# Kernel tuning notes

Hardware: AMD Instinct MI355X
Metric: run time of the kernel (lower is better)

The kernel has to match this reference:

```python
import jax, jax.numpy as jnp
import numpy as np

B, L, D_MODEL = 2, 2048, 512
EXPAND = 2
ED = EXPAND * D_MODEL          # d_inner = 1024
N = 16                          # d_state
D_CONV = 4
DT_RANK = (D_MODEL + N - 1) // N  # 32
D_FF = 1024
EPS = 1e-5


def _mamba_params(key, pre):
    ks = jax.random.split(key, 6)
    s = 0.02
    p = {}
    p[pre + 'in_w'] = jax.random.normal(ks[0], (D_MODEL, 2 * ED), jnp.float32) * s
    p[pre + 'conv_w'] = jax.random.normal(ks[1], (ED, 1, D_CONV), jnp.float32) * s
    p[pre + 'conv_b'] = jnp.zeros((ED,), jnp.float32)
    p[pre + 'xproj_w'] = jax.random.normal(ks[2], (ED, DT_RANK + 2 * N), jnp.float32) * s
    p[pre + 'dt_w'] = jax.random.normal(ks[3], (DT_RANK, ED), jnp.float32) * s
    p[pre + 'dt_b'] = jax.random.normal(ks[4], (ED,), jnp.float32) * s
    # S4D-real init: A_log = log(1..N) per channel
    p[pre + 'A_log'] = jnp.log(jnp.broadcast_to(jnp.arange(1, N + 1, dtype=jnp.float32), (ED, N)))
    p[pre + 'D'] = jnp.ones((ED,), jnp.float32)
    p[pre + 'out_w'] = jax.random.normal(ks[5], (ED, D_MODEL), jnp.float32) * s
    return p


def setup_inputs() -> dict:
    key = jax.random.key(0)
    k_x, k_f, k_b, k_ffn = jax.random.split(key, 4)
    inp = {'x': jax.random.normal(k_x, (B, L, D_MODEL), jnp.float32)}
    inp.update(_mamba_params(k_f, 'f_'))
    inp.update(_mamba_params(k_b, 'b_'))
    inp['norm1_g'] = jnp.ones((D_MODEL,), jnp.float32)
    inp['norm1_b'] = jnp.zeros((D_MODEL,), jnp.float32)
    inp['norm2_g'] = jnp.ones((D_MODEL,), jnp.float32)
    inp['norm2_b'] = jnp.zeros((D_MODEL,), jnp.float32)
    k1, k2 = jax.random.split(k_ffn)
    inp['ffn_w1'] = jax.random.normal(k1, (D_MODEL, D_FF), jnp.float32) * 0.02
    inp['ffn_b1'] = jnp.zeros((D_FF,), jnp.float32)
    inp['ffn_w2'] = jax.random.normal(k2, (D_FF, D_MODEL), jnp.float32) * 0.02
    inp['ffn_b2'] = jnp.zeros((D_MODEL,), jnp.float32)
    return inp


def _selective_scan(x, delta, A, Bm, C, Dp):
    # x, delta: (B,L,ED); A: (ED,N); Bm, C: (B,L,N); Dp: (ED,)
    def step(h, inp):
        x_t, d_t, B_t, C_t = inp  # (B,ED),(B,ED),(B,N),(B,N)
        dA = jnp.exp(d_t[..., None] * A)                      # (B,ED,N)
        dBx = (d_t * x_t)[..., None] * B_t[:, None, :]        # (B,ED,N)
        h = dA * h + dBx
        y = jnp.einsum('ben,bn->be', h, C_t)
        return h, y

    h0 = jnp.zeros((x.shape[0], ED, N), x.dtype)
    xs = (x.transpose(1, 0, 2), delta.transpose(1, 0, 2),
          Bm.transpose(1, 0, 2), C.transpose(1, 0, 2))
    _, ys = jax.lax.scan(step, h0, xs)
    return ys.transpose(1, 0, 2) + x * Dp


def _mamba(x, in_w, conv_w, conv_b, xproj_w, dt_w, dt_b, A_log, Dp, out_w):
    xz = x @ in_w                                  # (B,L,2*ED)
    xs, z = jnp.split(xz, 2, axis=-1)
    # depthwise causal conv over time
    xc = jax.lax.conv_general_dilated(
        xs.transpose(0, 2, 1), conv_w, (1,), [(D_CONV - 1, 0)],
        dimension_numbers=('NCH', 'OIH', 'NCH'), feature_group_count=ED)
    xc = jax.nn.silu(xc.transpose(0, 2, 1) + conv_b)          # (B,L,ED)
    dbl = xc @ xproj_w                                        # (B,L,DT_RANK+2N)
    dt = dbl[..., :DT_RANK]
    Bm = dbl[..., DT_RANK:DT_RANK + N]
    C = dbl[..., DT_RANK + N:]
    delta = jax.nn.softplus(dt @ dt_w + dt_b)                 # (B,L,ED)
    A = -jnp.exp(A_log)
    y = _selective_scan(xc, delta, A, Bm, C, Dp)
    y = y * jax.nn.silu(z)
    return y @ out_w


def _layernorm(h, g, b):
    mu = jnp.mean(h, axis=-1, keepdims=True)
    var = jnp.var(h, axis=-1, keepdims=True)
    return (h - mu) * jax.lax.rsqrt(var + EPS) * g + b


def _ffn(h, w1, b1, w2, b2):
    return jnp.maximum(h @ w1 + b1, 0.0) @ w2 + b2


def reference(x,
              f_in_w, f_conv_w, f_conv_b, f_xproj_w, f_dt_w, f_dt_b, f_A_log, f_D, f_out_w,
              b_in_w, b_conv_w, b_conv_b, b_xproj_w, b_dt_w, b_dt_b, b_A_log, b_D, b_out_w,
              norm1_g, norm1_b, norm2_g, norm2_b,
              ffn_w1, ffn_b1, ffn_w2, ffn_b2):
    mf = _mamba(x, f_in_w, f_conv_w, f_conv_b, f_xproj_w, f_dt_w, f_dt_b, f_A_log, f_D, f_out_w)
    mf = _layernorm(mf, norm1_g, norm1_b)
    out_f = _ffn(mf, ffn_w1, ffn_b1, ffn_w2, ffn_b2) + mf
    # NOTE: original code computes norm2 but then uses the UN-normalized
    # backward output (variable shadowing bug); we replicate that faithfully.
    mb = _mamba(jnp.flip(x, axis=1), b_in_w, b_conv_w, b_conv_b, b_xproj_w,
                b_dt_w, b_dt_b, b_A_log, b_D, b_out_w)
    out_b = _ffn(mb, ffn_w1, ffn_b1, ffn_w2, ffn_b2) + mb
    return out_f + out_b
```

## Files before the change

### kernel.cpp

```cpp
#include <hip/hip_runtime.h>
#include <hip/hip_bf16.h>
#include <math.h>


#define BD 2
#define LD 2048
#define DMODEL 512
#define EDIM 1024
#define NST 16
#define DTR 32
#define DFF 1024
#define MROWS (BD*LD)

typedef __hip_bfloat16 bf16;
typedef __bf16 bf16x8 __attribute__((ext_vector_type(8)));
typedef __bf16 bf16x4 __attribute__((ext_vector_type(4)));
typedef float  f32x4  __attribute__((ext_vector_type(4)));

__device__ __forceinline__ float sig_(float x) { return 1.f / (1.f + __expf(-x)); }

__device__ __forceinline__ void glds16(const void* g, void* l)
{
    __builtin_amdgcn_global_load_lds(
        (const __attribute__((address_space(1))) void*)g,
        (__attribute__((address_space(3))) void*)l, 16, 0, 0);
}

__global__ __launch_bounds__(256)
void prep_k(const float* __restrict__ x, bf16* __restrict__ xbf,
            const float* __restrict__ inw_f, const float* __restrict__ inw_b,
            bf16* __restrict__ inwT,
            const float* __restrict__ outw_f, const float* __restrict__ outw_b,
            bf16* __restrict__ outwT,
            const float* __restrict__ fw1, bf16* __restrict__ fw1T,
            const float* __restrict__ fw2, bf16* __restrict__ fw2T,
            const float* __restrict__ xp_f, const float* __restrict__ xp_b,
            bf16* __restrict__ xpT,
            const float* __restrict__ dtw_f, const float* __restrict__ dtw_b,
            bf16* __restrict__ dtwT)
{
    const int bid = blockIdx.x, tid = threadIdx.x;
    if (bid < 2048) {
        size_t i = (size_t)bid * 1024 + tid * 4;
        float4 v = *(const float4*)(x + i);
        bf16* o = xbf + i;
        o[0] = __float2bfloat16(v.x); o[1] = __float2bfloat16(v.y);
        o[2] = __float2bfloat16(v.z); o[3] = __float2bfloat16(v.w);
        return;
    }
    const float* W; bf16* WT; int R, C, cx, ry;
    if (bid < 4096) {
        int d = (bid - 2048) >> 10, t = (bid - 2048) & 1023;
        W = d ? inw_b : inw_f; WT = inwT + (size_t)d * 2048 * 512;
        R = 512; C = 2048; cx = t & 63; ry = t >> 6;
    } else if (bid < 5120) {
        int d = (bid - 4096) >> 9, t = (bid - 4096) & 511;
        W = d ? outw_b : outw_f; WT = outwT + (size_t)d * 512 * 1024;
        R = 1024; C = 512; cx = t & 15; ry = t >> 4;
    } else if (bid < 5632) {
        int t = bid - 5120; W = fw1; WT = fw1T; R = 512; C = 1024;
        cx = t & 31; ry = t >> 5;
    } else if (bid < 6144) {
        int t = bid - 5632; W = fw2; WT = fw2T; R = 1024; C = 512;
        cx = t & 15; ry = t >> 4;
    } else if (bid < 6272) {
        int d = (bid - 6144) >> 6, t = (bid - 6144) & 63;
        W = d ? xp_b : xp_f; WT = xpT + (size_t)d * 64 * 1024;
        R = 1024; C = 64; cx = t & 1; ry = t >> 1;
    } else {
        int d = (bid - 6272) >> 5, t = (bid - 6272) & 31;
        W = d ? dtw_b : dtw_f; WT = dtwT + (size_t)d * 1024 * DTR;
        R = 32; C = 1024; cx = t; ry = 0;
    }
    __shared__ float tt[32][33];
    const int c0 = cx * 32, r0 = ry * 32;
    const int col = tid & 31, rr = tid >> 5;
#pragma unroll
    for (int p = 0; p < 4; ++p)
        tt[p * 8 + rr][col] = W[(size_t)(r0 + p * 8 + rr) * C + c0 + col];
    __syncthreads();
#pragma unroll
    for (int p = 0; p < 4; ++p)
        WT[(size_t)(c0 + p * 8 + rr) * R + r0 + col] =
            __float2bfloat16(tt[col][p * 8 + rr]);
}

template<int BN, int MODE, bool FLIPD1, bool CATK>
__global__ __launch_bounds__(256)
void bgemm3_k(const bf16* __restrict__ A, size_t Astr, int lda,
              const bf16* __restrict__ BT, size_t Bstr, int ldb,
              const float* __restrict__ bias,
              bf16* __restrict__ Cb, size_t Cstr, int ldc,
              const bf16* __restrict__ mp, size_t mpStr,
              float* __restrict__ outp, int K)
{
    constexpr int BM = 128;
    constexpr int FRm = 4, FRn = BN / 32;
    constexpr int KH = DFF;
    __shared__ __align__(16) bf16 As[BM][32];
    __shared__ __align__(16) bf16 Bs[BN][32];
    const int tid = threadIdx.x;
    const int dir = blockIdx.z;
    const bool flip = FLIPD1 && (dir == 1);
    const bf16* Ad = A + (CATK ? (size_t)0 : (size_t)dir * Astr);
    const bf16* Bd = BT + (size_t)dir * Bstr;
    const int bm = blockIdx.y * BM, bn = blockIdx.x * BN;
    const int wave = tid >> 6, lane = tid & 63;
    const int wm = (wave >> 1) * 64, wn = (wave & 1) * (BN / 2);
    const int lm = lane & 15, lq = lane >> 4;
    const int lrow = lane >> 2, lcol = (lane & 3) * 8;
    f32x4 acc[FRm][FRn] = {};

    for (int k0 = 0; k0 < K; k0 += 32) {
        const bf16* Ab = Ad;
        int ka = k0;
        if (CATK && k0 >= KH) { Ab = A + Astr; ka = k0 - KH; }
        const int kb = CATK ? (k0 & (KH - 1)) : k0;
#pragma unroll
        for (int c = 0; c < 2; ++c) {
            int row = c * 64 + wave * 16 + lrow;
            int gm = bm + row;
            if (flip) gm = (gm & ~(LD - 1)) + (LD - 1 - (gm & (LD - 1)));
            glds16(Ab + (size_t)gm * lda + ka + lcol,
                   &As[c * 64 + wave * 16][0]);
        }
#pragma unroll
        for (int c = 0; c < BN / 64; ++c) {
            int row = c * 64 + wave * 16 + lrow;
            glds16(Bd + (size_t)(bn + row) * ldb + kb + lcol,
                   &Bs[c * 64 + wave * 16][0]);
        }
        __syncthreads();

        bf16x8 af[FRm], bfr[FRn];
#pragma unroll
        for (int i = 0; i < FRm; ++i)
            af[i] = *(const bf16x8*)&As[wm + 16 * i + lm][lq * 8];
#pragma unroll
        for (int j = 0; j < FRn; ++j)
            bfr[j] = *(const bf16x8*)&Bs[wn + 16 * j + lm][lq * 8];
#pragma unroll
        for (int i = 0; i < FRm; ++i)
#pragma unroll
            for (int j = 0; j < FRn; ++j)
                acc[i][j] = __builtin_amdgcn_mfma_f32_16x16x32_bf16(
                    af[i], bfr[j], acc[i][j], 0, 0, 0);
        __syncthreads();
    }

    bf16* Cd = (MODE == 5) ? nullptr : Cb + (size_t)dir * Cstr;
#pragma unroll
    for (int i = 0; i < FRm; ++i) {
#pragma unroll
        for (int j = 0; j < FRn; ++j) {
            int col = bn + wn + 16 * j + lm;
            float bv = (MODE == 2) ? bias[col]
                     : (MODE == 5) ? 2.f * bias[col] : 0.f;
#pragma unroll
            for (int r = 0; r < 4; ++r) {
                int row = bm + wm + 16 * i + lq * 4 + r;
                float v = acc[i][j][r] + bv;
                size_t idx = (size_t)row * ldc + col;
                if (MODE == 0)      Cd[idx] = __float2bfloat16(v);
                else if (MODE == 2) Cd[idx] = __float2bfloat16(fmaxf(v, 0.f));
                else {
                    float m2 = __bfloat162float(mp[idx])
                             + __bfloat162float(mp[mpStr + idx]);
                    outp[idx] = v + m2;
                }
            }
        }
    }
}

__global__ __launch_bounds__(256)
void zgate_k(const bf16* __restrict__ xbf, const bf16* __restrict__ inwT,
             const bf16* __restrict__ y2t_all, bf16* __restrict__ yrow_all)
{
    __shared__ __align__(16) bf16 As[64][40];
    __shared__ __align__(16) bf16 Bs[128][40];
    __shared__ __bf16 sy[64][130];
    const int tid = threadIdx.x;
    const int dir = blockIdx.z;
    const bf16* Bd = inwT + (size_t)dir * (2048 * 512) + (size_t)1024 * 512;
    const bf16* y2t = y2t_all + (size_t)dir * ((size_t)MROWS * EDIM);
    bf16* yrow = yrow_all + (size_t)dir * ((size_t)MROWS * EDIM);
    const int bm = blockIdx.y * 64, bn = blockIdx.x * 128;
    const int wave = tid >> 6, lane = tid & 63;
    const int wm = (wave >> 1) * 32, wn = (wave & 1) * 64;
    const int lm = lane & 15, lq = lane >> 4;
    f32x4 acc[2][4] = {};

    for (int k0 = 0; k0 < 512; k0 += 32) {
        {
            int row = tid >> 2, col = (tid & 3) * 8;
            int gm = bm + row;
            if (dir == 1) gm = (gm & ~(LD - 1)) + (LD - 1 - (gm & (LD - 1)));
            *(bf16x8*)&As[row][col] =
                *(const bf16x8*)(xbf + (size_t)gm * 512 + k0 + col);
        }
#pragma unroll
        for (int p = 0; p < 2; ++p) {
            int row = p * 64 + (tid >> 2), col = (tid & 3) * 8;
            *(bf16x8*)&Bs[row][col] =
                *(const bf16x8*)(Bd + (size_t)(bn + row) * 512 + k0 + col);
        }
        __syncthreads();
        bf16x8 af[2], bfr[4];
#pragma unroll
        for (int i = 0; i < 2; ++i)
            af[i] = *(const bf16x8*)&As[wm + 16 * i + lm][lq * 8];
#pragma unroll
        for (int j = 0; j < 4; ++j)
            bfr[j] = *(const bf16x8*)&Bs[wn + 16 * j + lm][lq * 8];
#pragma unroll
        for (int i = 0; i < 2; ++i)
#pragma unroll
            for (int j = 0; j < 4; ++j)
                acc[i][j] = __builtin_amdgcn_mfma_f32_16x16x32_bf16(
                    af[i], bfr[j], acc[i][j], 0, 0, 0);
        __syncthreads();
    }

    {
        const int b = bm >> 11, l0 = bm & (LD - 1);
        int e = tid >> 1, lh = (tid & 1) * 32;
        const bf16* yp = y2t + ((size_t)b * EDIM + bn + e) * LD + l0 + lh;
#pragma unroll
        for (int i = 0; i < 4; ++i) {
            bf16x8 v = *(const bf16x8*)(yp + i * 8);
#pragma unroll
            for (int j = 0; j < 8; ++j) sy[lh + i * 8 + j][e] = v[j];
        }
    }
    __syncthreads();
#pragma unroll
    for (int i = 0; i < 2; ++i) {
#pragma unroll
        for (int j = 0; j < 4; ++j) {
            int col = bn + wn + 16 * j + lm;
#pragma unroll
            for (int r = 0; r < 4; ++r) {
                int row = bm + wm + 16 * i + lq * 4 + r;
                float z = acc[i][j][r];
                float g = z * sig_(z);
                float y = (float)sy[(row - bm)][col - bn];
                yrow[(size_t)row * EDIM + col] = __float2bfloat16(g * y);
            }
        }
    }
}

__global__ __launch_bounds__(256)
void conv2_k(const bf16* __restrict__ xs2,
             const float* __restrict__ cw_f, const float* __restrict__ cb_f,
             const float* __restrict__ cw_b, const float* __restrict__ cb_b,
             bf16* __restrict__ xct2)
{
    __shared__ float sxs[67][65];
    __shared__ float sout[64][65];
    const int tid = threadIdx.x;
    const int dir = blockIdx.z;
    const bf16* xs = xs2 + (size_t)dir * ((size_t)MROWS * EDIM);
    const float* w  = dir ? cw_b : cw_f;
    const float* cb = dir ? cb_b : cb_f;
    bf16* xct = xct2 + (size_t)dir * ((size_t)MROWS * EDIM);
    const int e0 = blockIdx.x * 64;
    const int bl0 = blockIdx.y * 64;
    const int lloc0 = bl0 & (LD - 1);
    const int b = bl0 >> 11;
    {
        int c8 = (tid & 7) * 8;
#pragma unroll
        for (int i = 0; i < 3; ++i) {
            int hr = i * 32 + (tid >> 3);
            if (hr < 67) {
                int lr = lloc0 + hr - 3;
                if (lr >= 0) {
                    bf16x8 v = *(const bf16x8*)(xs +
                        (size_t)(bl0 + hr - 3) * EDIM + e0 + c8);
#pragma unroll
                    for (int j = 0; j < 8; ++j) sxs[hr][c8 + j] = (float)v[j];
                } else {
#pragma unroll
                    for (int j = 0; j < 8; ++j) sxs[hr][c8 + j] = 0.f;
                }
            }
        }
    }
    __syncthreads();
    {
        int lr4 = tid >> 6, e = tid & 63;
        float w0 = w[(e0 + e) * 4 + 0], w1 = w[(e0 + e) * 4 + 1];
        float w2 = w[(e0 + e) * 4 + 2], w3 = w[(e0 + e) * 4 + 3];
        float cbv = cb[e0 + e];
#pragma unroll
        for (int i = 0; i < 16; ++i) {
            int lr = i * 4 + lr4;
            float acc = cbv;
            acc = fmaf(sxs[lr + 0][e], w0, acc);
            acc = fmaf(sxs[lr + 1][e], w1, acc);
            acc = fmaf(sxs[lr + 2][e], w2, acc);
            acc = fmaf(sxs[lr + 3][e], w3, acc);
            sout[e][lr] = acc * sig_(acc);
        }
    }
    __syncthreads();
    {
        int l8 = (tid & 7) * 8;
#pragma unroll
        for (int i = 0; i < 2; ++i) {
            int er = i * 32 + (tid >> 3);
            bf16x8 o;
#pragma unroll
            for (int j = 0; j < 8; ++j) o[j] = (__bf16)sout[er][l8 + j];
            *(bf16x8*)(xct + ((size_t)b * EDIM + e0 + er) * LD + lloc0 + l8) = o;
        }
    }
}

__global__ __launch_bounds__(256)
void g2m_k(const bf16* __restrict__ xct2, const bf16* __restrict__ xpT2,
           float* __restrict__ dblt2, float* __restrict__ dbldt2)
{
    __shared__ float As[64][33];
    __shared__ __align__(16) bf16 Bs[64][32];
    __shared__ float sC[32][65];
    const int tid = threadIdx.x;
    const int dir = blockIdx.z;
    const bf16* xct = xct2 + (size_t)dir * ((size_t)MROWS * EDIM);
    const bf16* xpT = xpT2 + (size_t)dir * (64 * 1024);
    float* dblt = dblt2 + (size_t)dir * (2 * 64 * LD);
    float* dbldt = dbldt2 + (size_t)dir * (2 * 2048 * DTR);
    const int bm = blockIdx.y * 64;
    const int bB = bm >> 11, l0 = bm & (LD - 1);
    const int wave = tid >> 6, lane = tid & 63;
    const int wm = (wave >> 1) * 32, wn = (wave & 1) * 32;
    const int lm = lane & 15, lq = lane >> 4;
    const int er = tid >> 3, l8 = (tid & 7) * 8;
    f32x4 acc[2][2] = {};

    for (int k0 = 0; k0 < EDIM; k0 += 32) {
        glds16(xpT + (size_t)(wave * 16 + (lane >> 2)) * 1024 + k0 + (lane & 3) * 8,
               &Bs[wave * 16][0]);
        {
            bf16x8 v = *(const bf16x8*)(xct +
                ((size_t)bB * EDIM + k0 + er) * LD + l0 + l8);
#pragma unroll
            for (int j = 0; j < 8; ++j) As[l8 + j][er] = (float)v[j];
        }
        __syncthreads();
        bf16x8 af[2], bfr[2];
#pragma unroll
        for (int i = 0; i < 2; ++i) {
            int row = wm + 16 * i + lm;
#pragma unroll
            for (int j = 0; j < 8; ++j) af[i][j] = (__bf16)As[row][lq * 8 + j];
        }
#pragma unroll
        for (int j = 0; j < 2; ++j)
            bfr[j] = *(const bf16x8*)&Bs[wn + 16 * j + lm][lq * 8];
#pragma unroll
        for (int i = 0; i < 2; ++i)
#pragma unroll
            for (int j = 0; j < 2; ++j)
                acc[i][j] = __builtin_amdgcn_mfma_f32_16x16x32_bf16(
                    af[i], bfr[j], acc[i][j], 0, 0, 0);
        __syncthreads();
    }
    if (wn == 0) {
#pragma unroll
        for (int i = 0; i < 2; ++i)
#pragma unroll
            for (int j = 0; j < 2; ++j) {
                int col = 16 * j + lm;
#pragma unroll
                for (int r = 0; r < 4; ++r) {
                    int row = wm + 16 * i + lq * 4 + r;
                    dbldt[(size_t)(bB * 2048 + l0 + row) * DTR + col] =
                        acc[i][j][r];
                }
            }
    } else {
#pragma unroll
        for (int i = 0; i < 2; ++i)
#pragma unroll
            for (int j = 0; j < 2; ++j) {
                int col = 16 * j + lm;
#pragma unroll
                for (int r = 0; r < 4; ++r)
                    sC[col][wm + 16 * i + lq * 4 + r] = acc[i][j][r];
            }
    }
    __syncthreads();
    {
        int nr = tid >> 3, ll = (tid & 7) * 8;
        float4 v0 = *(const float4*)&sC[nr][ll];
        float4 v1 = *(const float4*)&sC[nr][ll + 4];
        float* d = dblt + (size_t)(bB * 64 + 32 + nr) * LD + l0 + ll;
        *(float4*)d = v0; *(float4*)(d + 4) = v1;
    }
}

__global__ __launch_bounds__(256)
void g3m_k(const float* __restrict__ dbldt2, const bf16* __restrict__ dtwT2,
           const float* __restrict__ dtb_f, const float* __restrict__ dtb_b,
           bf16* __restrict__ dltt2)
{
    __shared__ __align__(16) bf16 As[64][40];
    __shared__ __align__(16) bf16 Bs[64][32];
    __shared__ float sC[64][65];
    const int tid = threadIdx.x;
    const int dir = blockIdx.z;
    const float* Ap = dbldt2 + (size_t)dir * (2 * 2048 * DTR);
    const bf16* BT = dtwT2 + (size_t)dir * (1024 * DTR);
    const float* bias = dir ? dtb_b : dtb_f;
    bf16* dltt = dltt2 + (size_t)dir * ((size_t)MROWS * EDIM);
    const int bm = blockIdx.y * 64, bn = blockIdx.x * 64;
    const int bB = bm >> 11, l0 = bm & (LD - 1);
    const int wave = tid >> 6, lane = tid & 63;
    const int wm = (wave >> 1) * 32, wn = (wave & 1) * 32;
    const int lm = lane & 15, lq = lane >> 4;

    {
        int row = tid >> 2, c8 = (tid & 3) * 8;
        const float* p = Ap + (size_t)(bB * 2048 + l0 + row) * DTR + c8;
        float4 v0 = *(const float4*)p, v1 = *(const float4*)(p + 4);
        bf16x8 o;
        o[0]=(__bf16)v0.x; o[1]=(__bf16)v0.y; o[2]=(__bf16)v0.z; o[3]=(__bf16)v0.w;
        o[4]=(__bf16)v1.x; o[5]=(__bf16)v1.y; o[6]=(__bf16)v1.z; o[7]=(__bf16)v1.w;
        *(bf16x8*)&As[row][c8] = o;
    }
    glds16(BT + (size_t)(bn + wave * 16 + (lane >> 2)) * DTR + (lane & 3) * 8,
           &Bs[wave * 16][0]);
    __syncthreads();

    bf16x8 af[2], bfr[2];
#pragma unroll
    for (int i = 0; i < 2; ++i)
        af[i] = *(const bf16x8*)&As[wm + 16 * i + lm][lq * 8];
#pragma unroll
    for (int j = 0; j < 2; ++j)
        bfr[j] = *(const bf16x8*)&Bs[wn + 16 * j + lm][lq * 8];
    f32x4 acc[2][2] = {};
#pragma unroll
    for (int i = 0; i < 2; ++i)
#pragma unroll
        for (int j = 0; j < 2; ++j)
            acc[i][j] = __builtin_amdgcn_mfma_f32_16x16x32_bf16(
                af[i], bfr[j], acc[i][j], 0, 0, 0);

#pragma unroll
    for (int i = 0; i < 2; ++i)
#pragma unroll
        for (int j = 0; j < 2; ++j) {
            int col = wn + 16 * j + lm;
            float bv = bias[bn + col];
#pragma unroll
            for (int r = 0; r < 4; ++r) {
                int row = wm + 16 * i + lq * 4 + r;
                float v = acc[i][j][r] + bv;
                v = (v > 20.f) ? v : log1pf(__expf(v));
                sC[col][row] = v;
            }
        }
    __syncthreads();
    {
        int erow = tid >> 2, l16 = (tid & 3) * 16;
        bf16* d = dltt + ((size_t)bB * EDIM + bn + erow) * LD + l0 + l16;
#pragma unroll
        for (int h = 0; h < 2; ++h) {
            bf16x8 o;
#pragma unroll
            for (int j = 0; j < 8; ++j) o[j] = (__bf16)sC[erow][l16 + h * 8 + j];
            *(bf16x8*)(d + h * 8) = o;
        }
    }
}

__global__ __launch_bounds__(256)
void scan6_k(bf16* __restrict__ xct2, const bf16* __restrict__ dltt2,
             const float* __restrict__ dblt2,
             const float* __restrict__ alog_f, const float* __restrict__ alog_b,
             const float* __restrict__ dp_f, const float* __restrict__ dp_b)
{
    __shared__ float sA[NST];
    __shared__ float sWp[NST][4];
    __shared__ float sWs[NST][4];
    const int gid = blockIdx.x;
    const int dir = gid >> 11;
    const int bb  = (gid >> 10) & 1;
    const int e   = gid & (EDIM - 1);
    const float* A_log = dir ? alog_b : alog_f;
    const float* Dp    = dir ? dp_b   : dp_f;
    bf16* xct = xct2 + (size_t)dir * ((size_t)MROWS * EDIM);
    const bf16* dltt = dltt2 + (size_t)dir * ((size_t)MROWS * EDIM);
    const float* bt = dblt2 + (size_t)dir * (2 * 64 * LD) + (size_t)bb * 64 * LD;
    const int tid = threadIdx.x;
    const int wave = tid >> 6, lane = tid & 63;
    const size_t baset = ((size_t)bb * EDIM + e) * LD;
    const int l0 = tid * 8;

    if (tid < NST) sA[tid] = -__expf(A_log[e * NST + tid]);

    float xv[8], dv[8], dx[8];
    {
        bf16x8 xr = *(const bf16x8*)(xct + baset + l0);
        bf16x8 dr = *(const bf16x8*)(dltt + baset + l0);
#pragma unroll
        for (int j = 0; j < 8; ++j) { xv[j] = (float)xr[j]; dv[j] = (float)dr[j]; }
    }
#pragma unroll
    for (int j = 0; j < 8; ++j) dx[j] = dv[j] * xv[j];
    __syncthreads();

    float y[8] = {};
    for (int n = 0; n < NST; ++n) {
        const float An = sA[n];
        const float* Bp = bt + (size_t)(DTR + n) * LD + l0;
        const float* Cp = bt + (size_t)(DTR + NST + n) * LD + l0;
        float4 b0 = *(const float4*)Bp, b1 = *(const float4*)(Bp + 4);
        float4 c0 = *(const float4*)Cp, c1 = *(const float4*)(Cp + 4);
        float Br[8] = {b0.x,b0.y,b0.z,b0.w, b1.x,b1.y,b1.z,b1.w};
        float Cr[8] = {c0.x,c0.y,c0.z,c0.w, c1.x,c1.y,c1.z,c1.w};

        float S[8], P[8];
        float h = 0.f, pr = 1.f;
#pragma unroll
        for (int l = 0; l < 8; ++l) {
            float a = __expf(dv[l] * An);
            pr *= a;
            h = fmaf(a, h, dx[l] * Br[l]);
            P[l] = pr; S[l] = h;
        }

        float p = pr, s = h;
#pragma unroll
        for (int d = 1; d < 64; d <<= 1) {
            float pp = __shfl_up(p, d, 64);
            float sp = __shfl_up(s, d, 64);
            if (lane >= d) { s = fmaf(sp, p, s); p *= pp; }
        }
        if (lane == 63) { sWp[n][wave] = p; sWs[n][wave] = s; }
        __syncthreads();
        float Hoff = 0.f;
#pragma unroll
        for (int w = 0; w < 3; ++w)
            if (w < wave) Hoff = fmaf(sWp[n][w], Hoff, sWs[n][w]);
        float pprev = __shfl_up(p, 1, 64);
        float sprev = __shfl_up(s, 1, 64);
        float H = (lane == 0) ? Hoff : fmaf(pprev, Hoff, sprev);

#pragma unroll
        for (int l = 0; l < 8; ++l)
            y[l] = fmaf(Cr[l], fmaf(P[l], H, S[l]), y[l]);
    }

    const float Dv = Dp[e];
    bf16x8 o;
#pragma unroll
    for (int l = 0; l < 8; ++l) o[l] = (__bf16)fmaf(xv[l], Dv, y[l]);
    *(bf16x8*)(xct + baset + l0) = o;
}

__global__ __launch_bounds__(256)
void ln_k(bf16* __restrict__ m, const float* __restrict__ gg,
          const float* __restrict__ bb)
{
    int row = (blockIdx.x * 256 + threadIdx.x) >> 6;
    int lane = threadIdx.x & 63;
    bf16* r = m + (size_t)row * DMODEL;
    float v[8], s = 0.f, s2 = 0.f;
#pragma unroll
    for (int i = 0; i < 8; ++i) {
        v[i] = __bfloat162float(r[lane + 64 * i]);
        s += v[i]; s2 = fmaf(v[i], v[i], s2);
    }
#pragma unroll
    for (int off = 32; off >= 1; off >>= 1) {
        s  += __shfl_xor(s, off, 64);
        s2 += __shfl_xor(s2, off, 64);
    }
    float mu = s * (1.f / DMODEL);
    float var = s2 * (1.f / DMODEL) - mu * mu;
    float inv = rsqrtf(var + 1e-5f);
#pragma unroll
    for (int i = 0; i < 8; ++i)
        r[lane + 64 * i] = __float2bfloat16(
            (v[i] - mu) * inv * gg[lane + 64 * i] + bb[lane + 64 * i]);
}

__global__ void sentinel_k(float* __restrict__ o)
{
    int i = blockIdx.x * 256 + threadIdx.x;
    o[i] = 100.0f;
}

extern "C" void kernel_launch(void* const* d_in, const int* in_sizes, int n_in,
                              void* d_out, int out_size, void* d_ws, size_t ws_size,
                              hipStream_t stream)
{
    const float* x    = (const float*)d_in[0];
    const float* n1g  = (const float*)d_in[19];
    const float* n1b  = (const float*)d_in[20];
    const float* fw1  = (const float*)d_in[23];
    const float* fb1  = (const float*)d_in[24];
    const float* fw2  = (const float*)d_in[25];
    const float* fb2  = (const float*)d_in[26];
    float* out = (float*)d_out;

    const size_t MiB = 1024 * 1024;
    const size_t SZ_DM = (size_t)MROWS * DMODEL;
    if (ws_size < 49 * MiB) {
        sentinel_k<<<dim3(SZ_DM / 256), dim3(256), 0, stream>>>(out);
        return;
    }

    char* base = (char*)d_ws;
    bf16* fw1T  = (bf16*)base;
    bf16* fw2T  = (bf16*)(base + 1 * MiB);
    bf16* outwT = (bf16*)(base + 2 * MiB);
    bf16* inwT  = (bf16*)(base + 4 * MiB);
    bf16* xbf   = (bf16*)(base + 8 * MiB);
    char* RA    = base + 12 * MiB;
    bf16* xs2   = (bf16*)RA;
    bf16* dltt2 = (bf16*)RA;
    bf16* yrow2 = (bf16*)RA;
    bf16* ffh2  = (bf16*)RA;
    char* RB    = base + 28 * MiB;
    bf16* xct2  = (bf16*)RB;
    bf16* mbf2  = (bf16*)RB;
    float* dblt2 = (float*)(base + 44 * MiB);
    float* dbldt2 = (float*)(base + 46 * MiB);
    bf16* xpT2  = (bf16*)(base + 48 * MiB);
    bf16* dtwT2 = (bf16*)(base + 48 * MiB + 256 * 1024);

    const float* inw_f  = (const float*)d_in[1];
    const float* cw_f   = (const float*)d_in[2];
    const float* cb_f   = (const float*)d_in[3];
    const float* xp_f   = (const float*)d_in[4];
    const float* dtw_f  = (const float*)d_in[5];
    const float* dtb_f  = (const float*)d_in[6];
    const float* alog_f = (const float*)d_in[7];
    const float* dp_f   = (const float*)d_in[8];
    const float* outw_f = (const float*)d_in[9];
    const float* inw_b  = (const float*)d_in[10];
    const float* cw_b   = (const float*)d_in[11];
    const float* cb_b   = (const float*)d_in[12];
    const float* xp_b   = (const float*)d_in[13];
    const float* dtw_b  = (const float*)d_in[14];
    const float* dtb_b  = (const float*)d_in[15];
    const float* alog_b = (const float*)d_in[16];
    const float* dp_b   = (const float*)d_in[17];
    const float* outw_b = (const float*)d_in[18];

    dim3 blk(256);
    const size_t U = (size_t)MROWS * EDIM;

    prep_k<<<dim3(6336), blk, 0, stream>>>(x, xbf, inw_f, inw_b, inwT,
                                           outw_f, outw_b, outwT,
                                           fw1, fw1T, fw2, fw2T,
                                           xp_f, xp_b, xpT2,
                                           dtw_f, dtw_b, dtwT2);
    bgemm3_k<128, 0, true, false><<<dim3(8, 32, 2), blk, 0, stream>>>(
        xbf, 0, DMODEL, inwT, (size_t)2048 * 512, DMODEL, nullptr,
        xs2, U, EDIM, nullptr, 0, nullptr, DMODEL);
    conv2_k<<<dim3(16, 64, 2), blk, 0, stream>>>(xs2, cw_f, cb_f, cw_b, cb_b, xct2);
    g2m_k<<<dim3(1, 64, 2), blk, 0, stream>>>(xct2, xpT2, dblt2, dbldt2);
    g3m_k<<<dim3(16, 64, 2), blk, 0, stream>>>(dbldt2, dtwT2, dtb_f, dtb_b, dltt2);
    scan6_k<<<dim3(4096), blk, 0, stream>>>(xct2, dltt2, dblt2,
                                            alog_f, alog_b, dp_f, dp_b);
    zgate_k<<<dim3(8, 64, 2), blk, 0, stream>>>(xbf, inwT, xct2, yrow2);
    bgemm3_k<64, 0, false, false><<<dim3(8, 32, 2), blk, 0, stream>>>(
        yrow2, U, EDIM, outwT, (size_t)512 * 1024, EDIM, nullptr,
        mbf2, SZ_DM, DMODEL, nullptr, 0, nullptr, EDIM);
    ln_k<<<dim3(MROWS / 4), blk, 0, stream>>>(mbf2, n1g, n1b);
    bgemm3_k<128, 2, false, false><<<dim3(8, 32, 2), blk, 0, stream>>>(
        mbf2, SZ_DM, DMODEL, fw1T, 0, DMODEL, fb1,
        ffh2, U, DFF, nullptr, 0, nullptr, DMODEL);
    bgemm3_k<64, 5, false, true><<<dim3(8, 32, 1), blk, 0, stream>>>(
        ffh2, U, DFF, fw2T, 0, DFF, fb2,
        nullptr, 0, DMODEL, mbf2, SZ_DM, out, 2 * DFF);
}
```

Before: 372.2 us.

## Double GEMM K-tile to 64 and halve g2m row tile for more blocks

```diff
diff --git a/kernel.cpp b/kernel.cpp
--- a/kernel.cpp
+++ b/kernel.cpp
@@ -94,11 +94,11 @@
               const bf16* __restrict__ mp, size_t mpStr,
               float* __restrict__ outp, int K)
 {
-    constexpr int BM = 128;
+    constexpr int BM = 128, BK = 64;
     constexpr int FRm = 4, FRn = BN / 32;
     constexpr int KH = DFF;
-    __shared__ __align__(16) bf16 As[BM][32];
-    __shared__ __align__(16) bf16 Bs[BN][32];
+    __shared__ __align__(16) bf16 As[BM][BK];
+    __shared__ __align__(16) bf16 Bs[BN][BK];
     const int tid = threadIdx.x;
     const int dir = blockIdx.z;
     const bool flip = FLIPD1 && (dir == 1);
@@ -108,43 +108,46 @@
     const int wave = tid >> 6, lane = tid & 63;
     const int wm = (wave >> 1) * 64, wn = (wave & 1) * (BN / 2);
     const int lm = lane & 15, lq = lane >> 4;
-    const int lrow = lane >> 2, lcol = (lane & 3) * 8;
+    const int lrow = lane >> 3, lcol = (lane & 7) * 8;
     f32x4 acc[FRm][FRn] = {};
 
-    for (int k0 = 0; k0 < K; k0 += 32) {
+    for (int k0 = 0; k0 < K; k0 += BK) {
         const bf16* Ab = Ad;
         int ka = k0;
         if (CATK && k0 >= KH) { Ab = A + Astr; ka = k0 - KH; }
         const int kb = CATK ? (k0 & (KH - 1)) : k0;
 #pragma unroll
-        for (int c = 0; c < 2; ++c) {
-            int row = c * 64 + wave * 16 + lrow;
+        for (int c = 0; c < 4; ++c) {
+            int row = c * 32 + wave * 8 + lrow;
             int gm = bm + row;
             if (flip) gm = (gm & ~(LD - 1)) + (LD - 1 - (gm & (LD - 1)));
             glds16(Ab + (size_t)gm * lda + ka + lcol,
-                   &As[c * 64 + wave * 16][0]);
-        }
-#pragma unroll
-        for (int c = 0; c < BN / 64; ++c) {
-            int row = c * 64 + wave * 16 + lrow;
+                   &As[c * 32 + wave * 8][0]);
+        }
+#pragma unroll
+        for (int c = 0; c < BN / 32; ++c) {
+            int row = c * 32 + wave * 8 + lrow;
             glds16(Bd + (size_t)(bn + row) * ldb + kb + lcol,
-                   &Bs[c * 64 + wave * 16][0]);
+                   &Bs[c * 32 + wave * 8][0]);
         }
         __syncthreads();
 
-        bf16x8 af[FRm], bfr[FRn];
-#pragma unroll
-        for (int i = 0; i < FRm; ++i)
-            af[i] = *(const bf16x8*)&As[wm + 16 * i + lm][lq * 8];
-#pragma unroll
-        for (int j = 0; j < FRn; ++j)
-            bfr[j] = *(const bf16x8*)&Bs[wn + 16 * j + lm][lq * 8];
-#pragma unroll
-        for (int i = 0; i < FRm; ++i)
+#pragma unroll
+        for (int kh = 0; kh < 2; ++kh) {
+            bf16x8 af[FRm], bfr[FRn];
+#pragma unroll
+            for (int i = 0; i < FRm; ++i)
+                af[i] = *(const bf16x8*)&As[wm + 16 * i + lm][kh * 32 + lq * 8];
 #pragma unroll
             for (int j = 0; j < FRn; ++j)
-                acc[i][j] = __builtin_amdgcn_mfma_f32_16x16x32_bf16(
-                    af[i], bfr[j], acc[i][j], 0, 0, 0);
+                bfr[j] = *(const bf16x8*)&Bs[wn + 16 * j + lm][kh * 32 + lq * 8];
+#pragma unroll
+            for (int i = 0; i < FRm; ++i)
+#pragma unroll
+                for (int j = 0; j < FRn; ++j)
+                    acc[i][j] = __builtin_amdgcn_mfma_f32_16x16x32_bf16(
+                        af[i], bfr[j], acc[i][j], 0, 0, 0);
+        }
         __syncthreads();
     }
 
@@ -323,82 +326,73 @@
 void g2m_k(const bf16* __restrict__ xct2, const bf16* __restrict__ xpT2,
            float* __restrict__ dblt2, float* __restrict__ dbldt2)
 {
-    __shared__ float As[64][33];
+    __shared__ float As[32][33];
     __shared__ __align__(16) bf16 Bs[64][32];
-    __shared__ float sC[32][65];
+    __shared__ float sDT[32][33];
+    __shared__ float sBC[32][33];
     const int tid = threadIdx.x;
     const int dir = blockIdx.z;
     const bf16* xct = xct2 + (size_t)dir * ((size_t)MROWS * EDIM);
     const bf16* xpT = xpT2 + (size_t)dir * (64 * 1024);
     float* dblt = dblt2 + (size_t)dir * (2 * 64 * LD);
     float* dbldt = dbldt2 + (size_t)dir * (2 * 2048 * DTR);
-    const int bm = blockIdx.y * 64;
+    const int bm = blockIdx.y * 32;
     const int bB = bm >> 11, l0 = bm & (LD - 1);
     const int wave = tid >> 6, lane = tid & 63;
-    const int wm = (wave >> 1) * 32, wn = (wave & 1) * 32;
+    const int wml = (wave >> 1) * 16, wnn = (wave & 1) * 32;
     const int lm = lane & 15, lq = lane >> 4;
-    const int er = tid >> 3, l8 = (tid & 7) * 8;
-    f32x4 acc[2][2] = {};
+    const int er = tid >> 3, l4 = (tid & 7) * 4;
+    f32x4 acc[2] = {};
 
     for (int k0 = 0; k0 < EDIM; k0 += 32) {
         glds16(xpT + (size_t)(wave * 16 + (lane >> 2)) * 1024 + k0 + (lane & 3) * 8,
                &Bs[wave * 16][0]);
         {
-            bf16x8 v = *(const bf16x8*)(xct +
-                ((size_t)bB * EDIM + k0 + er) * LD + l0 + l8);
-#pragma unroll
-            for (int j = 0; j < 8; ++j) As[l8 + j][er] = (float)v[j];
+            bf16x4 v = *(const bf16x4*)(xct +
+                ((size_t)bB * EDIM + k0 + er) * LD + l0 + l4);
+#pragma unroll
+            for (int j = 0; j < 4; ++j) As[l4 + j][er] = (float)v[j];
         }
         __syncthreads();
-        bf16x8 af[2], bfr[2];
-#pragma unroll
-        for (int i = 0; i < 2; ++i) {
-            int row = wm + 16 * i + lm;
-#pragma unroll
-            for (int j = 0; j < 8; ++j) af[i][j] = (__bf16)As[row][lq * 8 + j];
-        }
-#pragma unroll
-        for (int j = 0; j < 2; ++j)
-            bfr[j] = *(const bf16x8*)&Bs[wn + 16 * j + lm][lq * 8];
-#pragma unroll
-        for (int i = 0; i < 2; ++i)
-#pragma unroll
-            for (int j = 0; j < 2; ++j)
-                acc[i][j] = __builtin_amdgcn_mfma_f32_16x16x32_bf16(
-                    af[i], bfr[j], acc[i][j], 0, 0, 0);
+        bf16x8 af;
+#pragma unroll
+        for (int j = 0; j < 8; ++j) af[j] = (__bf16)As[wml + lm][lq * 8 + j];
+#pragma unroll
+        for (int j = 0; j < 2; ++j) {
+            bf16x8 bfr = *(const bf16x8*)&Bs[wnn + 16 * j + lm][lq * 8];
+            acc[j] = __builtin_amdgcn_mfma_f32_16x16x32_bf16(af, bfr, acc[j], 0, 0, 0);
+        }
         __syncthreads();
     }
-    if (wn == 0) {
-#pragma unroll
-        for (int i = 0; i < 2; ++i)
-#pragma unroll
-            for (int j = 0; j < 2; ++j) {
-                int col = 16 * j + lm;
-#pragma unroll
-                for (int r = 0; r < 4; ++r) {
-                    int row = wm + 16 * i + lq * 4 + r;
-                    dbldt[(size_t)(bB * 2048 + l0 + row) * DTR + col] =
-                        acc[i][j][r];
-                }
-            }
+    if (wnn == 0) {
+#pragma unroll
+        for (int j = 0; j < 2; ++j) {
+            int col = 16 * j + lm;
+#pragma unroll
+            for (int r = 0; r < 4; ++r)
+                sDT[wml + lq * 4 + r][col] = acc[j][r];
+        }
     } else {
 #pragma unroll
-        for (int i = 0; i < 2; ++i)
-#pragma unroll
-            for (int j = 0; j < 2; ++j) {
-                int col = 16 * j + lm;
-#pragma unroll
-                for (int r = 0; r < 4; ++r)
-                    sC[col][wm + 16 * i + lq * 4 + r] = acc[i][j][r];
-            }
-    }
-    __syncthreads();
-    {
-        int nr = tid >> 3, ll = (tid & 7) * 8;
-        float4 v0 = *(const float4*)&sC[nr][ll];
-        float4 v1 = *(const float4*)&sC[nr][ll + 4];
-        float* d = dblt + (size_t)(bB * 64 + 32 + nr) * LD + l0 + ll;
-        *(float4*)d = v0; *(float4*)(d + 4) = v1;
+        for (int j = 0; j < 2; ++j) {
+            int col = 16 * j + lm;
+#pragma unroll
+            for (int r = 0; r < 4; ++r)
+                sBC[col][wml + lq * 4 + r] = acc[j][r];
+        }
+    }
+    __syncthreads();
+    {
+        int row = tid >> 3, c4 = (tid & 7) * 4;
+        float4 v = make_float4(sDT[row][c4], sDT[row][c4 + 1],
+                               sDT[row][c4 + 2], sDT[row][c4 + 3]);
+        *(float4*)(dbldt + (size_t)(bB * 2048 + l0 + row) * DTR + c4) = v;
+    }
+    {
+        int nr = tid >> 3, ll = (tid & 7) * 4;
+        float4 v = make_float4(sBC[nr][ll], sBC[nr][ll + 1],
+                               sBC[nr][ll + 2], sBC[nr][ll + 3]);
+        *(float4*)(dblt + (size_t)(bB * 64 + 32 + nr) * LD + l0 + ll) = v;
     }
 }
 
@@ -666,7 +660,7 @@
         xbf, 0, DMODEL, inwT, (size_t)2048 * 512, DMODEL, nullptr,
         xs2, U, EDIM, nullptr, 0, nullptr, DMODEL);
     conv2_k<<<dim3(16, 64, 2), blk, 0, stream>>>(xs2, cw_f, cb_f, cw_b, cb_b, xct2);
-    g2m_k<<<dim3(1, 64, 2), blk, 0, stream>>>(xct2, xpT2, dblt2, dbldt2);
+    g2m_k<<<dim3(1, 128, 2), blk, 0, stream>>>(xct2, xpT2, dblt2, dbldt2);
     g3m_k<<<dim3(16, 64, 2), blk, 0, stream>>>(dbldt2, dtwT2, dtb_f, dtb_b, dltt2);
     scan6_k<<<dim3(4096), blk, 0, stream>>>(xct2, dltt2, dblt2,
                                             alog_f, alog_b, dp_f, dp_b);
```

Result: faster. 358.5 us (-3.7%).
